# Optimization experiments

Hardware: AMD Instinct MI355X
Metric: run time of the kernel (lower is better)

## Reference

```python
import jax, jax.numpy as jnp
import numpy as np

H = 8          # attention heads
EPS = 1e-5     # LayerNorm eps (torch default)
B, T, E = 8, 1024, 128
D, DI, N, DC, R = 512, 1024, 16, 4, 32   # d_model, d_inner, d_state, d_conv, dt_rank
NT, NM = 6, 8                            # transformer layers, mamba layers
FF = 2048                                # transformer dim_feedforward (torch default)


def setup_inputs():
    key = jax.random.key(0)
    ks = iter(jax.random.split(key, 48))
    def rn(shape, scale=0.05):
        return jax.random.normal(next(ks), shape, jnp.float32) * scale
    return {
        "emb":      jax.random.normal(next(ks), (B, T, E), jnp.float32),
        # TransformerEncoder (6 post-norm layers), params stacked on leading layer dim
        "t_wqkv":   rn((NT, 3 * E, E)), "t_bqkv": jnp.zeros((NT, 3 * E), jnp.float32),
        "t_wo":     rn((NT, E, E)),     "t_bo":   jnp.zeros((NT, E), jnp.float32),
        "t_ln1w":   jnp.ones((NT, E), jnp.float32),  "t_ln1b": jnp.zeros((NT, E), jnp.float32),
        "t_w1":     rn((NT, FF, E)),    "t_b1":   jnp.zeros((NT, FF), jnp.float32),
        "t_w2":     rn((NT, E, FF)),    "t_b2":   jnp.zeros((NT, E), jnp.float32),
        "t_ln2w":   jnp.ones((NT, E), jnp.float32),  "t_ln2b": jnp.zeros((NT, E), jnp.float32),
        # Linear(emb_dim -> d_model)
        "w_in":     rn((D, E)), "b_in": jnp.zeros((D,), jnp.float32),
        # MambaBlocks (8 raw Mamba layers, no residual/norm), stacked
        "m_inproj": rn((NM, 2 * DI, D)),
        "m_convw":  rn((NM, DI, DC), 0.2), "m_convb": jnp.zeros((NM, DI), jnp.float32),
        "m_xproj":  rn((NM, R + 2 * N, DI)),
        "m_dtw":    rn((NM, DI, R), 0.1),
        "m_dtb":    jax.random.uniform(next(ks), (NM, DI), jnp.float32, -6.0, -3.0),
        "m_Alog":   jnp.log(jnp.tile(jnp.arange(1, N + 1, dtype=jnp.float32), (NM, DI, 1))),
        "m_D":      jnp.ones((NM, DI), jnp.float32),
        "m_outproj": rn((NM, D, DI)),
        # Linear(d_model -> emb_dim)
        "w_out":    rn((E, D)), "b_out": jnp.zeros((E,), jnp.float32),
    }


def _ln(x, w, b):
    mu = jnp.mean(x, -1, keepdims=True)
    var = jnp.var(x, -1, keepdims=True)
    return (x - mu) * jax.lax.rsqrt(var + EPS) * w + b


def _tlayer(x, p):
    wqkv, bqkv, wo, bo, ln1w, ln1b, w1, b1, w2, b2, ln2w, ln2b = p
    qkv = x @ wqkv.T + bqkv                        # (B,T,3E)
    q, k, v = jnp.split(qkv, 3, axis=-1)
    def heads(t):                                  # (B,T,E) -> (B,H,T,E//H)
        return t.reshape(B, T, H, E // H).transpose(0, 2, 1, 3)
    q, k, v = heads(q), heads(k), heads(v)
    scores = jnp.einsum("bhqd,bhkd->bhqk", q, k) / jnp.sqrt(jnp.float32(E // H))
    attn = jax.nn.softmax(scores, axis=-1)
    o = jnp.einsum("bhqk,bhkd->bhqd", attn, v).transpose(0, 2, 1, 3).reshape(B, T, E)
    x = _ln(x + o @ wo.T + bo, ln1w, ln1b)         # post-norm (torch default)
    ff = jax.nn.relu(x @ w1.T + b1) @ w2.T + b2
    return _ln(x + ff, ln2w, ln2b)


def _mamba_layer(x, p):
    inproj, convw, convb, xproj, dtw, dtb, Alog, Dp, outproj = p
    xz = x @ inproj.T                              # (B,T,2*DI)
    xi, z = jnp.split(xz, 2, axis=-1)
    # causal depthwise conv1d, kernel DC, left-padded
    xp = jnp.pad(xi, ((0, 0), (DC - 1, 0), (0, 0)))
    conv = sum(xp[:, k:k + T, :] * convw[:, k] for k in range(DC)) + convb
    xi = jax.nn.silu(conv)
    dbc = xi @ xproj.T                             # (B,T,R+2N)
    dt_r, Bt, Ct = dbc[..., :R], dbc[..., R:R + N], dbc[..., R + N:]
    dt = jax.nn.softplus(dt_r @ dtw.T + dtb)       # (B,T,DI)
    A = -jnp.exp(Alog)                             # (DI,N)
    def step(h, inputs):
        dt_t, B_t, C_t, x_t = inputs               # (B,DI),(B,N),(B,N),(B,DI)
        dA = jnp.exp(dt_t[:, :, None] * A)         # (B,DI,N)
        h = h * dA + (dt_t * x_t)[:, :, None] * B_t[:, None, :]
        y = jnp.einsum("bdn,bn->bd", h, C_t)
        return h, y
    h0 = jnp.zeros((B, DI, N), x.dtype)
    seq = (dt.transpose(1, 0, 2), Bt.transpose(1, 0, 2),
           Ct.transpose(1, 0, 2), xi.transpose(1, 0, 2))
    _, ys = jax.lax.scan(step, h0, seq)            # ys: (T,B,DI)
    y = ys.transpose(1, 0, 2) + Dp * xi
    y = y * jax.nn.silu(z)
    return y @ outproj.T                           # (B,T,D)


def reference(emb, t_wqkv, t_bqkv, t_wo, t_bo, t_ln1w, t_ln1b, t_w1, t_b1, t_w2, t_b2,
              t_ln2w, t_ln2b, w_in, b_in, m_inproj, m_convw, m_convb, m_xproj, m_dtw,
              m_dtb, m_Alog, m_D, m_outproj, w_out, b_out):
    x = emb
    tparams = (t_wqkv, t_bqkv, t_wo, t_bo, t_ln1w, t_ln1b, t_w1, t_b1, t_w2, t_b2, t_ln2w, t_ln2b)
    for i in range(NT):
        x = _tlayer(x, tuple(p[i] for p in tparams))
    x = x @ w_in.T + b_in                          # (B,T,D)
    mparams = (m_inproj, m_convw, m_convb, m_xproj, m_dtw, m_dtb, m_Alog, m_D, m_outproj)
    for i in range(NM):
        x = _mamba_layer(x, tuple(p[i] for p in mparams))
    return x @ w_out.T + b_out                     # (B,T,E)
```

## Files before the change

kernel.cpp:

```cpp
#include <hip/hip_runtime.h>
#include <math.h>

#define HB 8
#define TT 1024
#define NSTATE 16
#define NTT 6
#define NMM 8
#define MM (HB*TT)
#define EPSV 1e-5f
#define CHUNK 64
#define NCH (TT/CHUNK)
#define AKS 128
#define VST 136

typedef _Float16 f16x8 __attribute__((ext_vector_type(8)));
typedef _Float16 f16x4 __attribute__((ext_vector_type(4)));
typedef _Float16 f16x2 __attribute__((ext_vector_type(2)));
typedef float f32x4_t __attribute__((ext_vector_type(4)));

static __device__ __forceinline__ void split8(const float4 a, const float4 b,
                                              f16x8& h, f16x8& l)
{
  float x[8] = {a.x, a.y, a.z, a.w, b.x, b.y, b.z, b.w};
#pragma unroll
  for (int i = 0; i < 8; i++) {
    _Float16 hi = (_Float16)x[i];
    h[i] = hi;
    l[i] = (_Float16)(x[i] - (float)hi);
  }
}

static __device__ __forceinline__ void gload16(const _Float16* g, _Float16* l)
{
  __builtin_amdgcn_global_load_lds(
      (const __attribute__((address_space(1))) unsigned int*)g,
      (__attribute__((address_space(3))) unsigned int*)l, 16, 0, 0);
}

static __device__ __forceinline__ void store_split(_Float16* __restrict__ dst,
                                                   size_t row, int col, float v)
{
  const int cc = col & 31;
  const size_t o = ((size_t)(col >> 5) * MM + row) * 64
                 + (size_t)(((((cc >> 3) ^ ((int)row & 7)) * 8)) + (cc & 7));
  _Float16 hi = (_Float16)v;
  dst[o] = hi;
  dst[o ^ (size_t)32] = (_Float16)(v - (float)hi);
}

static __device__ __forceinline__ void store_split2(_Float16* __restrict__ dst,
                                                    size_t row, int col0,
                                                    float v0, float v1)
{
  const int cc = col0 & 31;
  const size_t o = ((size_t)(col0 >> 5) * MM + row) * 64
                 + (size_t)(((((cc >> 3) ^ ((int)row & 7)) * 8)) + (cc & 7));
  _Float16 h0 = (_Float16)v0, h1 = (_Float16)v1;
  f16x2 hp = {h0, h1};
  f16x2 lp = {(_Float16)(v0 - (float)h0), (_Float16)(v1 - (float)h1)};
  *(f16x2*)&dst[o] = hp;
  *(f16x2*)&dst[o ^ (size_t)32] = lp;
}

static __device__ __forceinline__ void split_item(
    const float* __restrict__ src, int lda, int rows,
    _Float16* __restrict__ dst, int item)
{
  const int m = item % rows;
  const int seg = item / rows;
  const float* s = src + (size_t)m * lda + seg * 32;
  _Float16* d = dst + (size_t)item * 64;
  const int swz = m & 7;
#pragma unroll
  for (int g = 0; g < 4; g++) {
    float4 x0 = *(const float4*)&s[g * 8];
    float4 x1 = *(const float4*)&s[g * 8 + 4];
    f16x8 h, l;
    split8(x0, x1, h, l);
    const int u = (g ^ swz) * 8;
    *(f16x8*)&d[u] = h;
    *(f16x8*)&d[u ^ 32] = l;
  }
}

__global__ __launch_bounds__(256) void split_k(
    const float* __restrict__ src, int lda, int rows,
    _Float16* __restrict__ dst)
{
  split_item(src, lda, rows, dst, blockIdx.x * 256 + threadIdx.x);
}

__global__ __launch_bounds__(256) void split3_k(
    const float* __restrict__ s0, int lda0, int rows0, _Float16* __restrict__ d0, int nb0,
    const float* __restrict__ s1, int lda1, int rows1, _Float16* __restrict__ d1, int nb1,
    const float* __restrict__ s2, int lda2, int rows2, _Float16* __restrict__ d2)
{
  const int bid = blockIdx.x;
  if (bid < nb0) {
    split_item(s0, lda0, rows0, d0, bid * 256 + threadIdx.x);
  } else if (bid < nb0 + nb1) {
    split_item(s1, lda1, rows1, d1, (bid - nb0) * 256 + threadIdx.x);
  } else {
    split_item(s2, lda2, rows2, d2, (bid - nb0 - nb1) * 256 + threadIdx.x);
  }
}

__global__ __launch_bounds__(256) void split6_k(
    const float* __restrict__ s0, int lda0, int rows0, _Float16* __restrict__ d0, int c0,
    const float* __restrict__ s1, int lda1, int rows1, _Float16* __restrict__ d1, int c1,
    const float* __restrict__ s2, int lda2, int rows2, _Float16* __restrict__ d2, int c2,
    const float* __restrict__ s3, int lda3, int rows3, _Float16* __restrict__ d3, int c3,
    const float* __restrict__ s4, int lda4, int rows4, _Float16* __restrict__ d4, int c4,
    const float* __restrict__ s5, int lda5, int rows5, _Float16* __restrict__ d5)
{
  const int bid = blockIdx.x;
  if (bid < c0)      split_item(s0, lda0, rows0, d0, bid * 256 + threadIdx.x);
  else if (bid < c1) split_item(s1, lda1, rows1, d1, (bid - c0) * 256 + threadIdx.x);
  else if (bid < c2) split_item(s2, lda2, rows2, d2, (bid - c1) * 256 + threadIdx.x);
  else if (bid < c3) split_item(s3, lda3, rows3, d3, (bid - c2) * 256 + threadIdx.x);
  else if (bid < c4) split_item(s4, lda4, rows4, d4, (bid - c3) * 256 + threadIdx.x);
  else               split_item(s5, lda5, rows5, d5, (bid - c4) * 256 + threadIdx.x);
}

__global__ __launch_bounds__(256) void kv_split_k(
    const float* __restrict__ qkv,
    _Float16* __restrict__ Ks, _Float16* __restrict__ Vs)
{
  __shared__ _Float16 Vthi[16 * VST], Vtlo[16 * VST];
  const int tid = threadIdx.x;
  const int bh = blockIdx.y;
  const int b = bh >> 3;
  const int h = bh & 7;
  const int kb0 = blockIdx.x * 128;

  const int kl = tid >> 1;
  const int half = tid & 1;
  const int key = kb0 + kl;
  const float* kp = qkv + (size_t)(b * TT + key) * 384 + 128 + h * 16 + half * 8;

  {
    float4 k0 = *(const float4*)&kp[0];
    float4 k1 = *(const float4*)&kp[4];
    f16x8 hh, ll;
    split8(k0, k1, hh, ll);
    const int p = (half + (key >> 1)) & 3;
    _Float16* kb = Ks + (((size_t)bh << 10) + key) * 32;
    *(f16x8*)&kb[p * 8] = hh;
    *(f16x8*)&kb[(p ^ 2) * 8] = ll;
  }
  {
    float4 v0 = *(const float4*)&kp[128];
    float4 v1 = *(const float4*)&kp[132];
    float xv[8] = {v0.x, v0.y, v0.z, v0.w, v1.x, v1.y, v1.z, v1.w};
#pragma unroll
    for (int j = 0; j < 8; j++) {
      const int d = half * 8 + j;
      _Float16 hi = (_Float16)xv[j];
      Vthi[d * VST + kl] = hi;
      Vtlo[d * VST + kl] = (_Float16)(xv[j] - (float)hi);
    }
  }
  __syncthreads();
  {
    const int d = tid >> 4;
    const int kg = tid & 15;
    f16x8 hh = *(const f16x8*)&Vthi[d * VST + kg * 8];
    f16x8 ll = *(const f16x8*)&Vtlo[d * VST + kg * 8];
    _Float16* vb = Vs + ((size_t)bh * 32 + d) * 1024 + kb0 + ((kg ^ d) * 8);
    *(f16x8*)&vb[0] = hh;
    *(f16x8*)&vb[16 * 1024] = ll;
  }
}

template<int TN>
__global__ __launch_bounds__(256, 4) void gemm_ps_t(
    const _Float16* __restrict__ Ap, int astr,
    const _Float16* __restrict__ Wp, int wstr,
    const float* __restrict__ bias,
    float* __restrict__ C,
    float* __restrict__ P,
    _Float16* __restrict__ Cs,
    int N, int K, int S, int act)
{
  __shared__ __align__(16) _Float16 As[128 * 64];
  __shared__ __align__(16) _Float16 Bs[TN * 64];
  const int tid = threadIdx.x;
  const int lane = tid & 63;
  const int w = tid >> 6;
  const int quad = lane >> 4;
  const int l16 = lane & 15;

  const int gx = N / TN;
  const int bid = blockIdx.x;
  const int xcd = bid & 7;
  const int i = bid >> 3;
  const int iq = i / gx;
  const int by = xcd * 8 + iq;
  const int bx = i - iq * gx;

  const int m0 = by * 128;
  const int n0 = bx * TN;
  const int z = blockIdx.z;
  const int nseg = K / 32;
  const int segb = z * (nseg / S);
  const int sege = segb + nseg / S;

  constexpr int MI = (TN == 128) ? 4 : 2;
  const int w0 = (TN == 128) ? (w & 1) : w;
  const int w1 = (TN == 128) ? (w >> 1) : 0;
  const int rowbase = (TN == 128) ? w0 * 64 : w0 * 32;

  f32x4_t acc[MI][4];
#pragma unroll
  for (int i2 = 0; i2 < MI; i2++)
#pragma unroll
    for (int j = 0; j < 4; j++)
#pragma unroll
      for (int r = 0; r < 4; r++) acc[i2][j][r] = 0.f;

  const int sw8 = (quad ^ (l16 & 7)) * 8;
  const int abase = (rowbase + l16) * 64 + sw8;
  const int bbase = (w1 * 64 + l16) * 64 + sw8;
  const int wave64 = tid & 192;

  for (int seg = segb; seg < sege; seg++) {
    const _Float16* At = Ap + ((size_t)seg * astr + m0) * 64;
    const _Float16* Bt = Wp + ((size_t)seg * wstr + n0) * 64;
    __syncthreads();
#pragma unroll
    for (int j = 0; j < 4; j++)
      gload16(At + (size_t)(j * 256 + tid) * 8, &As[(j * 256 + wave64) * 8]);
#pragma unroll
    for (int j = 0; j < TN / 32; j++)
      gload16(Bt + (size_t)(j * 256 + tid) * 8, &Bs[(j * 256 + wave64) * 8]);
    __syncthreads();

    f16x8 bh[4], bl[4];
#pragma unroll
    for (int ni = 0; ni < 4; ni++) {
      bh[ni] = *(const f16x8*)&Bs[bbase + ni * 1024];
      bl[ni] = *(const f16x8*)&Bs[(bbase ^ 32) + ni * 1024];
    }
#pragma unroll
    for (int mi = 0; mi < MI; mi++) {
      f16x8 ah = *(const f16x8*)&As[abase + mi * 1024];
      f16x8 al = *(const f16x8*)&As[(abase ^ 32) + mi * 1024];
#pragma unroll
      for (int ni = 0; ni < 4; ni++) {
        acc[mi][ni] = __builtin_amdgcn_mfma_f32_16x16x32_f16(ah, bh[ni], acc[mi][ni], 0, 0, 0);
        acc[mi][ni] = __builtin_amdgcn_mfma_f32_16x16x32_f16(ah, bl[ni], acc[mi][ni], 0, 0, 0);
        acc[mi][ni] = __builtin_amdgcn_mfma_f32_16x16x32_f16(al, bh[ni], acc[mi][ni], 0, 0, 0);
      }
    }
  }

  float* dst = (S == 1) ? C : (P + (size_t)z * MM * N);
#pragma unroll
  for (int ni = 0; ni < 4; ni++) {
    const int n = n0 + w1 * 64 + ni * 16 + l16;
    const float bv = (S == 1 && bias) ? bias[n] : 0.f;
#pragma unroll
    for (int mi = 0; mi < MI; mi++) {
      const int mbase = m0 + rowbase + mi * 16 + quad * 4;
#pragma unroll
      for (int r = 0; r < 4; r++) {
        float v = acc[mi][ni][r] + bv;
        if (S == 1) {
          if (act == 1) v = fmaxf(v, 0.f);
          else if (act == 2) v = fmaxf(v, 0.f) + log1pf(__expf(-fabsf(v)));
        }
        const int row = mbase + r;
        if (S == 1 && Cs) {
          store_split(Cs, (size_t)row, n, v);
        } else {
          dst[(size_t)row * N + n] = v;
        }
      }
    }
  }
}

__global__ __launch_bounds__(256) void reduce_k(
    const float* __restrict__ P, const float* __restrict__ bias,
    float* __restrict__ C, _Float16* __restrict__ Cs,
    _Float16* __restrict__ dta,
    int nmask, int nshift, int S, int act, int stride4)
{
  const int idx = blockIdx.x * 256 + threadIdx.x;
  float4 a = *(const float4*)&P[(size_t)idx * 4];
  for (int z = 1; z < S; z++) {
    float4 p = *(const float4*)&P[(size_t)(idx + (size_t)z * stride4) * 4];
    a.x += p.x; a.y += p.y; a.z += p.z; a.w += p.w;
  }
  if (bias) {
    float4 bv = *(const float4*)&bias[(idx * 4) & nmask];
    a.x += bv.x; a.y += bv.y; a.z += bv.z; a.w += bv.w;
  }
  if (act == 1) {
    a.x = fmaxf(a.x, 0.f); a.y = fmaxf(a.y, 0.f);
    a.z = fmaxf(a.z, 0.f); a.w = fmaxf(a.w, 0.f);
  } else if (act == 2) {
    a.x = fmaxf(a.x, 0.f) + log1pf(__expf(-fabsf(a.x)));
    a.y = fmaxf(a.y, 0.f) + log1pf(__expf(-fabsf(a.y)));
    a.z = fmaxf(a.z, 0.f) + log1pf(__expf(-fabsf(a.z)));
    a.w = fmaxf(a.w, 0.f) + log1pf(__expf(-fabsf(a.w)));
  }
  const int c0 = (idx * 4) & nmask;
  const size_t row = (size_t)(idx * 4) >> nshift;
  if (Cs) {
    store_split2(Cs, row, c0,     a.x, a.y);
    store_split2(Cs, row, c0 + 2, a.z, a.w);
  } else {
    *(float4*)&C[(size_t)idx * 4] = a;
  }
  if (dta && c0 < 32) {
    store_split2(dta, row, c0,     a.x, a.y);
    store_split2(dta, row, c0 + 2, a.z, a.w);
  }
}

__global__ __launch_bounds__(256) void attn_mfma_k(
    const float* __restrict__ qkv,
    const _Float16* __restrict__ Kg,
    const _Float16* __restrict__ Vg,
    _Float16* __restrict__ os)
{
  __shared__ __align__(16) _Float16 Klds[AKS * 32];
  __shared__ __align__(16) _Float16 Vlds[32 * AKS];
  __shared__ float Pscr[4][16 * 18];

  const int tid = threadIdx.x;
  const int lane = tid & 63;
  const int wv = tid >> 6;
  const int quad = lane >> 4;
  const int l16 = lane & 15;
  const int qh = quad & 1;
  const int bh = blockIdx.y;
  const int b = bh >> 3;
  const int h = bh & 7;
  const int qb0 = blockIdx.x * 128;
  const int wave64 = tid & 192;

  f16x8 qa[2];
#pragma unroll
  for (int u = 0; u < 2; u++) {
    const int qrow = qb0 + wv * 32 + u * 16 + l16;
    const float* qp = qkv + (size_t)(b * TT + qrow) * 384 + h * 16 + qh * 8;
    float4 x0 = *(const float4*)&qp[0];
    float4 x1 = *(const float4*)&qp[4];
    float xv[8] = {x0.x, x0.y, x0.z, x0.w, x1.x, x1.y, x1.z, x1.w};
#pragma unroll
    for (int j = 0; j < 8; j++) {
      float q = xv[j] * 0.25f;
      _Float16 hi = (_Float16)q;
      _Float16 lo = (_Float16)(q - (float)hi);
      qa[u][j] = (quad < 2) ? hi : lo;
    }
  }

  f32x4_t oacc[2];
  float lacc[2][4];
#pragma unroll
  for (int u = 0; u < 2; u++)
#pragma unroll
    for (int r = 0; r < 4; r++) { oacc[u][r] = 0.f; lacc[u][r] = 0.f; }

  float* Pw = &Pscr[wv][0];
  const _Float16* Kb = Kg + (((size_t)bh) << 10) * 32;
  const _Float16* Vb = Vg + ((size_t)bh * 32) * 1024;

  for (int ks = 0; ks < TT; ks += AKS) {
    __syncthreads();
    {
      const _Float16* Kt = Kb + (size_t)ks * 32;
#pragma unroll
      for (int it = 0; it < 2; it++) {
        const int cb = it * 256 + tid;
        gload16(Kt + (size_t)cb * 8, &Klds[(it * 256 + wave64) * 8]);
      }
#pragma unroll
      for (int it = 0; it < 2; it++) {
        const int cb = it * 256 + tid;
        const int rowv = cb >> 4, co = cb & 15;
        gload16(Vb + (size_t)rowv * 1024 + ks + co * 8,
                &Vlds[(it * 256 + wave64) * 8]);
      }
    }
    __syncthreads();

    for (int kt = 0; kt < AKS; kt += 16) {
      const int key = kt + l16;
      const int ph = (qh + (key >> 1)) & 3;
      f16x8 kfh = *(const f16x8*)&Klds[key * 32 + ph * 8];
      f16x8 kfl = *(const f16x8*)&Klds[key * 32 + (ph ^ 2) * 8];
      const int vko = (kt + qh * 8) ^ (l16 * 8);
      f16x8 vfh = *(const f16x8*)&Vlds[l16 * 128 + vko];
      f16x8 vfl = *(const f16x8*)&Vlds[(16 + l16) * 128 + vko];

#pragma unroll
      for (int u = 0; u < 2; u++) {
        f32x4_t s;
#pragma unroll
        for (int r = 0; r < 4; r++) s[r] = 0.f;
        s = __builtin_amdgcn_mfma_f32_16x16x32_f16(qa[u], kfh, s, 0, 0, 0);
        s = __builtin_amdgcn_mfma_f32_16x16x32_f16(qa[u], kfl, s, 0, 0, 0);
        float p[4];
#pragma unroll
        for (int r = 0; r < 4; r++) {
          p[r] = __expf(s[r]);
          lacc[u][r] += p[r];
        }
        float* ps = Pw + (quad * 4) * 18 + l16;
        ps[0] = p[0]; ps[18] = p[1]; ps[36] = p[2]; ps[54] = p[3];
        __asm__ volatile("s_waitcnt lgkmcnt(0)" ::: "memory");
        const float* pr = Pw + l16 * 18 + qh * 8;
        f16x8 pa;
#pragma unroll
        for (int j = 0; j < 8; j++) {
          float pv = pr[j];
          _Float16 hi = (_Float16)pv;
          _Float16 lo = (_Float16)(pv - (float)hi);
          pa[j] = (quad < 2) ? hi : lo;
        }
        oacc[u] = __builtin_amdgcn_mfma_f32_16x16x32_f16(pa, vfh, oacc[u], 0, 0, 0);
        oacc[u] = __builtin_amdgcn_mfma_f32_16x16x32_f16(pa, vfl, oacc[u], 0, 0, 0);
        __asm__ volatile("s_waitcnt lgkmcnt(0)" ::: "memory");
      }
    }
  }

#pragma unroll
  for (int u = 0; u < 2; u++) {
#pragma unroll
    for (int r = 0; r < 4; r++) {
      float lv = lacc[u][r];
      lv += __shfl_xor(lv, 1);
      lv += __shfl_xor(lv, 2);
      lv += __shfl_xor(lv, 4);
      lv += __shfl_xor(lv, 8);
      const float inv = 1.f / lv;
      const int qrow = qb0 + wv * 32 + u * 16 + quad * 4 + r;
      const size_t m = (size_t)(b * TT + qrow);
      store_split(os, m, h * 16 + l16, oacc[u][r] * inv);
    }
  }
}

__global__ __launch_bounds__(256) void add_ln_k(
    const float* __restrict__ a, const float* __restrict__ bvec,
    const float* __restrict__ w, const float* __restrict__ bb,
    float* __restrict__ out, _Float16* __restrict__ outs)
{
  const int tid = threadIdx.x;
  const int wave = tid >> 6, lane = tid & 63;
  const size_t row = (size_t)blockIdx.x * 4 + wave;
  const float* pa = a + row * 128;
  const float* pb = bvec + row * 128;
  float v0 = pa[lane] + pb[lane];
  float v1 = pa[lane + 64] + pb[lane + 64];
  float s1 = v0 + v1, s2 = v0 * v0 + v1 * v1;
#pragma unroll
  for (int off = 32; off; off >>= 1) {
    s1 += __shfl_down(s1, off);
    s2 += __shfl_down(s2, off);
  }
  s1 = __shfl(s1, 0); s2 = __shfl(s2, 0);
  const float mean = s1 * (1.f / 128.f);
  const float var = s2 * (1.f / 128.f) - mean * mean;
  const float rs = rsqrtf(var + EPSV);
  const float o0 = (v0 - mean) * rs * w[lane] + bb[lane];
  const float o1 = (v1 - mean) * rs * w[lane + 64] + bb[lane + 64];
  out[row * 128 + lane] = o0;
  out[row * 128 + lane + 64] = o1;
  store_split(outs, row, lane, o0);
  store_split(outs, row, lane + 64, o1);
}

__global__ __launch_bounds__(256) void conv_silu_k(
    const float* __restrict__ xz, const float* __restrict__ cw,
    const float* __restrict__ cb, float* __restrict__ out,
    _Float16* __restrict__ outs)
{
  const int idx = blockIdx.x * 256 + threadIdx.x;
  const int di = (idx & 511) * 2;
  const int tg = idx >> 9;
  const int m0 = tg * 4;
  const int t0 = m0 & (TT - 1);

  float wa[4], wb[4];
#pragma unroll
  for (int k = 0; k < 4; k++) {
    wa[k] = cw[di * 4 + k];
    wb[k] = cw[di * 4 + 4 + k];
  }
  const float b0 = cb[di], b1 = cb[di + 1];

  float2 xr[7];
#pragma unroll
  for (int j = 0; j < 7; j++) {
    if (t0 + j - 3 >= 0) {
      xr[j] = *(const float2*)&xz[(size_t)(m0 + j - 3) * 2048 + di];
    } else {
      xr[j].x = 0.f; xr[j].y = 0.f;
    }
  }

#pragma unroll
  for (int j = 0; j < 4; j++) {
    float a0 = b0, a1 = b1;
#pragma unroll
    for (int k = 0; k < 4; k++) {
      a0 += xr[j + k].x * wa[k];
      a1 += xr[j + k].y * wb[k];
    }
    const float y0 = a0 / (1.f + __expf(-a0));
    const float y1 = a1 / (1.f + __expf(-a1));
    float2 yo = {y0, y1};
    const size_t m = (size_t)(m0 + j);
    *(float2*)&out[m * 1024 + di] = yo;
    store_split2(outs, m, di, y0, y1);
  }
}

__global__ __launch_bounds__(64) void scan_partial_k(
    const float* __restrict__ dt,
    const float* __restrict__ dbc,
    const float* __restrict__ xi,
    const float* __restrict__ Alog,
    float* __restrict__ Pb, float* __restrict__ Sb)
{
  const int slice = blockIdx.x & 15;
  const int c = blockIdx.x >> 4;
  const int b = blockIdx.y;
  const int di = slice * 64 + threadIdx.x;

  float A[NSTATE];
#pragma unroll
  for (int n = 0; n < NSTATE; n++) A[n] = -__expf(Alog[di * NSTATE + n]);
  float h[NSTATE], P[NSTATE];
#pragma unroll
  for (int n = 0; n < NSTATE; n++) { h[n] = 0.f; P[n] = 1.f; }

  const size_t m0 = (size_t)b * TT + (size_t)c * CHUNK;
  for (int t = 0; t < CHUNK; t++) {
    const size_t m = m0 + t;
    const float dtv = dt[m * 1024 + di];
    const float xv  = xi[m * 1024 + di];
    const float dtx = dtv * xv;
#pragma unroll
    for (int n = 0; n < NSTATE; n++) {
      const float Bv = dbc[m * 64 + 32 + n];
      const float dA = __expf(dtv * A[n]);
      h[n] = h[n] * dA + dtx * Bv;
      P[n] *= dA;
    }
  }
  const size_t base = (((size_t)b * NCH + c) * NSTATE) * 1024 + di;
#pragma unroll
  for (int n = 0; n < NSTATE; n++) {
    Pb[base + (size_t)n * 1024] = P[n];
    Sb[base + (size_t)n * 1024] = h[n];
  }
}

__global__ __launch_bounds__(256) void scan_fix_k(
    float* __restrict__ Pb, const float* __restrict__ Sb)
{
  const int idx = blockIdx.x * 256 + threadIdx.x;
  const int di = idx & 1023;
  const int n  = (idx >> 10) & 15;
  const int b  = idx >> 14;
  float h = 0.f;
  for (int c = 0; c < NCH; c++) {
    const size_t base = (((size_t)b * NCH + c) * NSTATE + n) * 1024 + di;
    const float P = Pb[base];
    const float S = Sb[base];
    Pb[base] = h;
    h = P * h + S;
  }
}

__global__ __launch_bounds__(64) void scan_final_k(
    const float* __restrict__ dt,
    const float* __restrict__ dbc,
    const float* __restrict__ xi,
    const float* __restrict__ xz,
    const float* __restrict__ Alog,
    const float* __restrict__ Dp,
    const float* __restrict__ Hin,
    _Float16* __restrict__ Y)
{
  const int slice = blockIdx.x & 15;
  const int c = blockIdx.x >> 4;
  const int b = blockIdx.y;
  const int di = slice * 64 + threadIdx.x;

  float A[NSTATE];
#pragma unroll
  for (int n = 0; n < NSTATE; n++) A[n] = -__expf(Alog[di * NSTATE + n]);
  const float Dv = Dp[di];
  float h[NSTATE];
  const size_t hbase = (((size_t)b * NCH + c) * NSTATE) * 1024 + di;
#pragma unroll
  for (int n = 0; n < NSTATE; n++) h[n] = Hin[hbase + (size_t)n * 1024];

  const size_t m0 = (size_t)b * TT + (size_t)c * CHUNK;
  for (int t = 0; t < CHUNK; t++) {
    const size_t m = m0 + t;
    const float dtv = dt[m * 1024 + di];
    const float xv  = xi[m * 1024 + di];
    const float zv  = xz[m * 2048 + 1024 + di];
    const float dtx = dtv * xv;
    float y = 0.f;
#pragma unroll
    for (int n = 0; n < NSTATE; n++) {
      const float Bv = dbc[m * 64 + 32 + n];
      const float Cv = dbc[m * 64 + 48 + n];
      const float dA = __expf(dtv * A[n]);
      h[n] = h[n] * dA + dtx * Bv;
      y += h[n] * Cv;
    }
    y += Dv * xv;
    y *= zv / (1.f + __expf(-zv));
    store_split(Y, m, di, y);
  }
}

extern "C" void kernel_launch(void* const* d_in, const int* in_sizes, int n_in,
                              void* d_out, int out_size, void* d_ws, size_t ws_size,
                              hipStream_t stream)
{
  (void)in_sizes; (void)n_in; (void)out_size; (void)ws_size;
  const float* emb      = (const float*)d_in[0];
  const float* t_wqkv   = (const float*)d_in[1];
  const float* t_bqkv   = (const float*)d_in[2];
  const float* t_wo     = (const float*)d_in[3];
  const float* t_bo     = (const float*)d_in[4];
  const float* t_ln1w   = (const float*)d_in[5];
  const float* t_ln1b   = (const float*)d_in[6];
  const float* t_w1     = (const float*)d_in[7];
  const float* t_b1     = (const float*)d_in[8];
  const float* t_w2     = (const float*)d_in[9];
  const float* t_b2     = (const float*)d_in[10];
  const float* t_ln2w   = (const float*)d_in[11];
  const float* t_ln2b   = (const float*)d_in[12];
  const float* w_in     = (const float*)d_in[13];
  const float* b_in     = (const float*)d_in[14];
  const float* m_inproj = (const float*)d_in[15];
  const float* m_convw  = (const float*)d_in[16];
  const float* m_convb  = (const float*)d_in[17];
  const float* m_xproj  = (const float*)d_in[18];
  const float* m_dtw    = (const float*)d_in[19];
  const float* m_dtb    = (const float*)d_in[20];
  const float* m_Alog   = (const float*)d_in[21];
  const float* m_D      = (const float*)d_in[22];
  const float* m_outproj= (const float*)d_in[23];
  const float* w_out    = (const float*)d_in[24];
  const float* b_out    = (const float*)d_in[25];

  float* ws = (float*)d_ws;
  float* R1 = ws;
  float* R2 = ws + (size_t)MM * 512;
  float* R3 = ws + (size_t)MM * 1024;
  float* R4 = ws + (size_t)MM * 3072;
  float* R5 = ws + (size_t)MM * 4096;
  float* R6 = ws + (size_t)MM * 5120;
  float* R7 = ws + (size_t)MM * 6144;

  _Float16* TWQKV = (_Float16*)R4;
  _Float16* TWO   = TWQKV + (size_t)294912 * 2;
  _Float16* TW1   = TWO   + (size_t)98304 * 2;
  _Float16* TW2   = TW1   + (size_t)1572864 * 2;
  _Float16* TWIN  = TW2   + (size_t)1572864 * 2;

  _Float16* ASP1 = (_Float16*)R6;
  _Float16* XIS  = (_Float16*)R6;
  _Float16* DTA  = (_Float16*)R6;
  _Float16* YSP  = (_Float16*)R6;

  _Float16* KG = (_Float16*)(R2 + (size_t)MM * 256);
  _Float16* VG = (_Float16*)(R2 + (size_t)MM * 320);

  dim3 blk(256);
  auto split = [&](const float* src, int lda, int rows, int K, _Float16* dst) {
    hipLaunchKernelGGL(split_k, dim3(rows * (K / 32) / 256), blk, 0, stream,
                       src, lda, rows, dst);
  };
  auto gemm = [&](const _Float16* Ap, const _Float16* Wp, int wstr,
                  const float* bias, float* C, int N, int K, int act,
                  int S, float* P, _Float16* Cs, _Float16* dta, bool tn64) {
    dim3 g((N / (tn64 ? 64 : 128)) * (MM / 128), 1, S);
    if (tn64)
      hipLaunchKernelGGL(gemm_ps_t<64>, g, blk, 0, stream,
                         Ap, MM, Wp, wstr, bias, C, P, Cs, N, K, S, act);
    else
      hipLaunchKernelGGL(gemm_ps_t<128>, g, blk, 0, stream,
                         Ap, MM, Wp, wstr, bias, C, P, Cs, N, K, S, act);
    if (S > 1) {
      int stride4 = (int)((size_t)MM * N / 4);
      hipLaunchKernelGGL(reduce_k, dim3(stride4 / 256), blk, 0, stream,
                         P, bias, C, Cs, dta, N - 1, __builtin_ctz(N), S, act,
                         stride4);
    }
  };

  hipLaunchKernelGGL(split6_k, dim3(568), blk, 0, stream,
      t_wqkv, 128,  2304, TWQKV,  36,
      t_wo,   128,   768, TWO,    48,
      t_w1,   128, 12288, TW1,   240,
      t_w2,  2048,   768, TW2,   432,
      w_in,   128,   512, TWIN,  440,
      emb,    128,    MM, ASP1);

  const float* x = emb;
  for (int l = 0; l < NTT; l++) {
    gemm(ASP1, TWQKV + (size_t)l * 384 * 64, 2304, t_bqkv + l * 384,
         R3, 384, 128, 0, 1, nullptr, nullptr, nullptr, false);
    hipLaunchKernelGGL(kv_split_k, dim3(8, HB * 8), blk, 0, stream,
                       R3, KG, VG);
    hipLaunchKernelGGL(attn_mfma_k, dim3(TT / 128, HB * 8), blk, 0, stream,
                       R3, KG, VG, ASP1);
    gemm(ASP1, TWO + (size_t)l * 128 * 64, 768, t_bo + l * 128,
         R5, 128, 128, 0, 2, R2, nullptr, nullptr, true);
    hipLaunchKernelGGL(add_ln_k, dim3(MM / 4), blk, 0, stream,
                       x, R5, t_ln1w + l * 128, t_ln1b + l * 128, R1, ASP1);
    gemm(ASP1, TW1 + (size_t)l * 2048 * 64, 12288, t_b1 + l * 2048,
         R3, 2048, 128, 1, 1, nullptr, (_Float16*)R3, nullptr, false);
    gemm((_Float16*)R3, TW2 + (size_t)l * 128 * 64, 768, t_b2 + l * 128,
         R5, 128, 2048, 0, 8, R6, nullptr, nullptr, false);
    hipLaunchKernelGGL(add_ln_k, dim3(MM / 4), blk, 0, stream,
                       R1, R5, t_ln2w + l * 128, t_ln2b + l * 128, R1, ASP1);
    x = R1;
  }

  gemm(ASP1, TWIN, 512, b_in, R2, 512, 128, 0, 1, nullptr, (_Float16*)R2,
       nullptr, false);

  float* xcs = R2;
  float* xos = R1;
  for (int l = 0; l < NMM; l++) {
    _Float16* WIs = (_Float16*)(xos + (size_t)MM * 256);
    _Float16* WXs = (_Float16*)(xos + (size_t)MM * 384);
    _Float16* WDs = (_Float16*)(xos + (size_t)MM * 392);
    _Float16* WOs = (_Float16*)(xos + (size_t)MM * 256);
    hipLaunchKernelGGL(split3_k, dim3(140), blk, 0, stream,
        m_inproj + (size_t)l * 2048 * 512, 512, 2048, WIs, 128,
        m_xproj  + (size_t)l * 64 * 1024, 1024,   64, WXs,   8,
        m_dtw    + (size_t)l * 1024 * 32,   32, 1024, WDs);

    gemm((_Float16*)xcs, WIs, 2048, nullptr,
         R3, 2048, 512, 0, 1, nullptr, nullptr, nullptr, false);
    hipLaunchKernelGGL(conv_silu_k, dim3(MM / 2), blk, 0, stream,
                       R3, m_convw + (size_t)l * 1024 * 4, m_convb + l * 1024,
                       R4, XIS);
    gemm(XIS, WXs, 64, nullptr,
         R7, 64, 1024, 0, 4, xos, nullptr, DTA, true);
    gemm(DTA, WDs, 1024, m_dtb + l * 1024,
         R5, 1024, 32, 2, 1, nullptr, nullptr, nullptr, false);

    float* Pb = xos;
    float* Sb = xos + (size_t)MM * 256;
    hipLaunchKernelGGL(scan_partial_k, dim3(16 * NCH, HB), dim3(64), 0, stream,
                       R5, R7, R4, m_Alog + (size_t)l * 1024 * 16, Pb, Sb);
    hipLaunchKernelGGL(scan_fix_k, dim3(HB * NSTATE * 1024 / 256), blk, 0,
                       stream, Pb, Sb);
    split(m_outproj + (size_t)l * 512 * 1024, 1024, 512, 1024, WOs);
    hipLaunchKernelGGL(scan_final_k, dim3(16 * NCH, HB), dim3(64), 0, stream,
                       R5, R7, R4, R3,
                       m_Alog + (size_t)l * 1024 * 16, m_D + l * 1024, Pb, YSP);

    gemm(YSP, WOs, 512, nullptr,
         R5, 512, 1024, 0, 2, R3, (_Float16*)xos, nullptr, false);
    float* ts = xcs; xcs = xos; xos = ts;
  }

  _Float16* WOUTs = (_Float16*)xos;
  split(w_out, 512, 128, 512, WOUTs);
  gemm((_Float16*)xcs, WOUTs, 128, b_out,
       (float*)d_out, 128, 512, 0, 4, R6, nullptr, nullptr, false);
}
```

Measured before the change: 3.356 ms.

## Restructure attention kernel: 64-query blocks, transposed S MFMA, shuffle-based P transpose

The attention kernel now handles 64 queries per block (16 per wave) instead of 128, which doubles the grid. It computes S transposed by swapping the MFMA operands, so the P fragment can be rebuilt with lane shuffles instead of an LDS scratch round-trip with explicit waitcnts. The row-sum is accumulated per column and reduced once at the end. It also adds s_setprio around MFMAs and an occupancy hint of 4 blocks. The cost is that each block reloads K/V from global memory for fewer queries, which doubles K/V traffic.

New measurement: 4.213 ms. +25.5%, slower.

```diff
diff --git a/kernel.cpp b/kernel.cpp
--- a/kernel.cpp
+++ b/kernel.cpp
@@ -319,7 +319,7 @@
   }
 }
 
-__global__ __launch_bounds__(256) void attn_mfma_k(
+__global__ __launch_bounds__(256, 4) void attn_mfma_k(
     const float* __restrict__ qkv,
     const _Float16* __restrict__ Kg,
     const _Float16* __restrict__ Vg,
@@ -327,7 +327,6 @@
 {
   __shared__ __align__(16) _Float16 Klds[AKS * 32];
   __shared__ __align__(16) _Float16 Vlds[32 * AKS];
-  __shared__ float Pscr[4][16 * 18];
 
   const int tid = threadIdx.x;
   const int lane = tid & 63;
@@ -338,13 +337,12 @@
   const int bh = blockIdx.y;
   const int b = bh >> 3;
   const int h = bh & 7;
-  const int qb0 = blockIdx.x * 128;
+  const int qb0 = blockIdx.x * 64;
   const int wave64 = tid & 192;
 
-  f16x8 qa[2];
-#pragma unroll
-  for (int u = 0; u < 2; u++) {
-    const int qrow = qb0 + wv * 32 + u * 16 + l16;
+  f16x8 qa;
+  {
+    const int qrow = qb0 + wv * 16 + l16;
     const float* qp = qkv + (size_t)(b * TT + qrow) * 384 + h * 16 + qh * 8;
     float4 x0 = *(const float4*)&qp[0];
     float4 x1 = *(const float4*)&qp[4];
@@ -354,18 +352,17 @@
       float q = xv[j] * 0.25f;
       _Float16 hi = (_Float16)q;
       _Float16 lo = (_Float16)(q - (float)hi);
-      qa[u][j] = (quad < 2) ? hi : lo;
-    }
-  }
-
-  f32x4_t oacc[2];
-  float lacc[2][4];
-#pragma unroll
-  for (int u = 0; u < 2; u++)
-#pragma unroll
-    for (int r = 0; r < 4; r++) { oacc[u][r] = 0.f; lacc[u][r] = 0.f; }
-
-  float* Pw = &Pscr[wv][0];
+      qa[j] = (quad < 2) ? hi : lo;
+    }
+  }
+
+  f32x4_t oacc;
+  float dch[8];
+#pragma unroll
+  for (int r = 0; r < 4; r++) oacc[r] = 0.f;
+#pragma unroll
+  for (int j = 0; j < 8; j++) dch[j] = 0.f;
+
   const _Float16* Kb = Kg + (((size_t)bh) << 10) * 32;
   const _Float16* Vb = Vg + ((size_t)bh * 32) * 1024;
 
@@ -397,52 +394,47 @@
       f16x8 vfh = *(const f16x8*)&Vlds[l16 * 128 + vko];
       f16x8 vfl = *(const f16x8*)&Vlds[(16 + l16) * 128 + vko];
 
-#pragma unroll
-      for (int u = 0; u < 2; u++) {
-        f32x4_t s;
-#pragma unroll
-        for (int r = 0; r < 4; r++) s[r] = 0.f;
-        s = __builtin_amdgcn_mfma_f32_16x16x32_f16(qa[u], kfh, s, 0, 0, 0);
-        s = __builtin_amdgcn_mfma_f32_16x16x32_f16(qa[u], kfl, s, 0, 0, 0);
-        float p[4];
-#pragma unroll
-        for (int r = 0; r < 4; r++) {
-          p[r] = __expf(s[r]);
-          lacc[u][r] += p[r];
-        }
-        float* ps = Pw + (quad * 4) * 18 + l16;
-        ps[0] = p[0]; ps[18] = p[1]; ps[36] = p[2]; ps[54] = p[3];
-        __asm__ volatile("s_waitcnt lgkmcnt(0)" ::: "memory");
-        const float* pr = Pw + l16 * 18 + qh * 8;
-        f16x8 pa;
-#pragma unroll
-        for (int j = 0; j < 8; j++) {
-          float pv = pr[j];
-          _Float16 hi = (_Float16)pv;
-          _Float16 lo = (_Float16)(pv - (float)hi);
-          pa[j] = (quad < 2) ? hi : lo;
-        }
-        oacc[u] = __builtin_amdgcn_mfma_f32_16x16x32_f16(pa, vfh, oacc[u], 0, 0, 0);
-        oacc[u] = __builtin_amdgcn_mfma_f32_16x16x32_f16(pa, vfl, oacc[u], 0, 0, 0);
-        __asm__ volatile("s_waitcnt lgkmcnt(0)" ::: "memory");
+      f32x4_t s;
+#pragma unroll
+      for (int r = 0; r < 4; r++) s[r] = 0.f;
+      __builtin_amdgcn_s_setprio(1);
+      s = __builtin_amdgcn_mfma_f32_16x16x32_f16(kfh, qa, s, 0, 0, 0);
+      s = __builtin_amdgcn_mfma_f32_16x16x32_f16(kfl, qa, s, 0, 0, 0);
+      __builtin_amdgcn_s_setprio(0);
+
+      float p[4];
+#pragma unroll
+      for (int r = 0; r < 4; r++) p[r] = __expf(s[r]);
+
+      f16x8 pa;
+#pragma unroll
+      for (int j = 0; j < 8; j++) {
+        const float pv = __shfl(p[j & 3], ((qh * 2 + (j >> 2)) << 4) + l16);
+        dch[j] += pv;
+        _Float16 hi = (_Float16)pv;
+        _Float16 lo = (_Float16)(pv - (float)hi);
+        pa[j] = (quad < 2) ? hi : lo;
       }
-    }
-  }
-
-#pragma unroll
-  for (int u = 0; u < 2; u++) {
-#pragma unroll
-    for (int r = 0; r < 4; r++) {
-      float lv = lacc[u][r];
-      lv += __shfl_xor(lv, 1);
-      lv += __shfl_xor(lv, 2);
-      lv += __shfl_xor(lv, 4);
-      lv += __shfl_xor(lv, 8);
-      const float inv = 1.f / lv;
-      const int qrow = qb0 + wv * 32 + u * 16 + quad * 4 + r;
-      const size_t m = (size_t)(b * TT + qrow);
-      store_split(os, m, h * 16 + l16, oacc[u][r] * inv);
-    }
+
+      __builtin_amdgcn_s_setprio(1);
+      oacc = __builtin_amdgcn_mfma_f32_16x16x32_f16(pa, vfh, oacc, 0, 0, 0);
+      oacc = __builtin_amdgcn_mfma_f32_16x16x32_f16(pa, vfl, oacc, 0, 0, 0);
+      __builtin_amdgcn_s_setprio(0);
+    }
+  }
+
+  const float e0 = dch[0] + dch[1], e1 = dch[2] + dch[3];
+  const float e2 = dch[4] + dch[5], e3 = dch[6] + dch[7];
+  const float g = (e0 + e1) + (e2 + e3);
+  const float lv = g + __shfl_xor(g, 16);
+
+#pragma unroll
+  for (int r = 0; r < 4; r++) {
+    const float dq = __shfl(lv, quad * 4 + r);
+    const float inv = 1.f / dq;
+    const int qrow = qb0 + wv * 16 + quad * 4 + r;
+    const size_t m = (size_t)(b * TT + qrow);
+    store_split(os, m, h * 16 + l16, oacc[r] * inv);
   }
 }
 
@@ -718,7 +710,7 @@
          R3, 384, 128, 0, 1, nullptr, nullptr, nullptr, false);
     hipLaunchKernelGGL(kv_split_k, dim3(8, HB * 8), blk, 0, stream,
                        R3, KG, VG);
-    hipLaunchKernelGGL(attn_mfma_k, dim3(TT / 128, HB * 8), blk, 0, stream,
+    hipLaunchKernelGGL(attn_mfma_k, dim3(TT / 64, HB * 8), blk, 0, stream,
                        R3, KG, VG, ASP1);
     gemm(ASP1, TWO + (size_t)l * 128 * 64, 768, t_bo + l * 128,
          R5, 128, 128, 0, 2, R2, nullptr, nullptr, true);
```
